# Kernel optimization log

Measured on AMD Instinct MI355X. Metric: run time of the kernel, lower is better.

The kernel has to match this reference:

```python
import jax, jax.numpy as jnp
import numpy as np

GROUPS = 3
EPS = 1e-5

def _conv(x, w, groups, pad):
    # x: NCHW, w: OIHW (grouped). pad: 'VALID' for 1x1, ((1,1),(1,1)) for 3x3 same.
    return jax.lax.conv_general_dilated(
        x, w, window_strides=(1, 1), padding=pad,
        feature_group_count=groups,
        dimension_numbers=('NCHW', 'OIHW', 'NCHW'))

def _bn(x, g, b, m, v):
    # folded inference batchnorm: y = x*scale + (beta - mean*scale)
    s = g / jnp.sqrt(v + EPS)
    return x * s[None, :, None, None] + (b - m * s)[None, :, None, None]

def _shuffle(x, groups):
    B, C, H, W = x.shape
    return x.reshape(B, groups, C // groups, H, W).transpose(0, 2, 1, 3, 4).reshape(B, C, H, W)

def setup_inputs() -> dict:
    key = jax.random.key(0)
    ks = jax.random.split(key, 16)
    B, Cin, Cout, H, W = 64, 480, 480, 28, 28
    mid = Cout // 4  # 120
    d = {}
    d['x'] = jax.random.normal(ks[0], (B, Cin, H, W), jnp.float32)
    d['w1'] = jax.random.normal(ks[1], (mid, Cin // GROUPS, 1, 1), jnp.float32) * 0.05
    d['g1'] = jax.random.uniform(ks[2], (mid,), jnp.float32)
    d['b1'] = jax.random.normal(ks[3], (mid,), jnp.float32)
    d['m1'] = jax.random.normal(ks[4], (mid,), jnp.float32)
    d['v1'] = jax.random.uniform(ks[5], (mid,), jnp.float32)
    d['w2'] = jax.random.normal(ks[6], (mid, 1, 3, 3), jnp.float32) * 0.05
    d['g2'] = jax.random.uniform(ks[7], (mid,), jnp.float32)
    d['b2'] = jax.random.normal(ks[8], (mid,), jnp.float32)
    d['m2'] = jax.random.normal(ks[9], (mid,), jnp.float32)
    d['v2'] = jax.random.uniform(ks[10], (mid,), jnp.float32)
    d['w3'] = jax.random.normal(ks[11], (Cout, mid // GROUPS, 1, 1), jnp.float32) * 0.05
    d['g3'] = jax.random.uniform(ks[12], (Cout,), jnp.float32)
    d['b3'] = jax.random.normal(ks[13], (Cout,), jnp.float32)
    d['m3'] = jax.random.normal(ks[14], (Cout,), jnp.float32)
    d['v3'] = jax.random.uniform(ks[15], (Cout,), jnp.float32)
    return d

def reference(x, w1, g1, b1, m1, v1, w2, g2, b2, m2, v2, w3, g3, b3, m3, v3):
    mid = w2.shape[0]
    shortcut = x  # in_channels == out_channels -> identity shortcut
    out = jax.nn.relu(_bn(_conv(x, w1, GROUPS, 'VALID'), g1, b1, m1, v1))
    out = _bn(_conv(out, w2, mid, ((1, 1), (1, 1))), g2, b2, m2, v2)  # depthwise 3x3
    out = _shuffle(out, GROUPS)
    out = jax.nn.relu(_bn(_conv(out, w3, GROUPS, 'VALID'), g3, b3, m3, v3))
    return out + shortcut
```

## Files before the change

### kernel.cpp

```cpp
#include <hip/hip_runtime.h>


namespace {
constexpr int CIN = 480;
constexpr int MID = 120;
constexpr int HWP = 784;
constexpr float EPSV = 1e-5f;

constexpr size_t TMP1_N   = (size_t)64 * MID * HWP;
constexpr size_t G_SHORTS = (size_t)784 * 3 * 4096;
constexpr size_t G_FLOATS = G_SHORTS / 2;
constexpr size_t PAR_OFF  = TMP1_N + G_FLOATS;
constexpr int WA1_N = 3 * 3 * 5 * 64 * 8;
constexpr int WA3_N = 3 * 10 * 2 * 64 * 8;

constexpr int S1X = 161;
constexpr int S2O = 69;
constexpr int S3O = 67;
}

typedef short bf16x8 __attribute__((ext_vector_type(8)));
typedef float f32x4  __attribute__((ext_vector_type(4)));

__device__ inline unsigned short f2bf(float v) {
    unsigned u = __float_as_uint(v);
    return (unsigned short)((u + 0x7fffu + ((u >> 16) & 1u)) >> 16);
}
__device__ inline float bf2f(unsigned short s) {
    return __uint_as_float(((unsigned)s) << 16);
}
__device__ inline void split2(float v, unsigned short& h, unsigned short& l) {
    h = f2bf(v);
    l = f2bf(v - bf2f(h));
}

__global__ __launch_bounds__(256) void prep_k(
    const float* __restrict__ w1, const float* __restrict__ w3,
    const float* __restrict__ g1, const float* __restrict__ b1,
    const float* __restrict__ m1, const float* __restrict__ v1,
    const float* __restrict__ g2, const float* __restrict__ b2,
    const float* __restrict__ m2, const float* __restrict__ v2,
    const float* __restrict__ g3, const float* __restrict__ b3,
    const float* __restrict__ m3, const float* __restrict__ v3,
    float* __restrict__ par, unsigned short* __restrict__ wpk,
    unsigned short* __restrict__ G)
{
    const int t = blockIdx.x * 256 + threadIdx.x;
    if (t < 720) {
        if (t < 120) {
            const float s = g1[t] * rsqrtf(v1[t] + EPSV);
            par[t] = s; par[120 + t] = fmaf(-m1[t], s, b1[t]);
        } else if (t < 240) {
            const int c = t - 120;
            const float s = g2[c] * rsqrtf(v2[c] + EPSV);
            par[240 + c] = s; par[360 + c] = fmaf(-m2[c], s, b2[c]);
        } else {
            const int c = t - 240;
            const float s = g3[c] * rsqrtf(v3[c] + EPSV);
            par[480 + c] = s; par[960 + c] = fmaf(-m3[c], s, b3[c]);
        }
    } else if (t < 3600) {
        const int t1   = t - 720;
        const int lane = t1 & 63;
        const int rest = t1 >> 6;
        const int ks   = rest % 5;
        const int mtg  = rest / 5;
        const int mt   = mtg % 3;
        const int g    = mtg / 3;
        const int row  = mt * 16 + (lane & 15);
        const int k0   = ks * 32 + (lane >> 4) * 8;
        unsigned short h[8], l[8];
#pragma unroll
        for (int j = 0; j < 8; ++j) {
            float v = (row < 40) ? w1[(size_t)(g * 40 + row) * 160 + k0 + j] : 0.f;
            split2(v, h[j], l[j]);
        }
        *reinterpret_cast<uint4*>(wpk + (size_t)t1 * 8)         = *reinterpret_cast<uint4*>(h);
        *reinterpret_cast<uint4*>(wpk + WA1_N + (size_t)t1 * 8) = *reinterpret_cast<uint4*>(l);
    } else if (t < 7440) {
        const int t3   = t - 3600;
        const int lane = t3 & 63;
        const int rest = t3 >> 6;
        const int ks   = rest % 2;
        const int mtg  = rest / 2;
        const int mt   = mtg % 10;
        const int g    = mtg / 10;
        const int row  = mt * 16 + (lane & 15);
        const int k0   = ks * 32 + (lane >> 4) * 8;
        unsigned short h[8], l[8];
#pragma unroll
        for (int j = 0; j < 8; ++j) {
            const int k = k0 + j;
            float v = (k < 40) ? w3[(size_t)(g * 160 + row) * 40 + k] : 0.f;
            split2(v, h[j], l[j]);
        }
        *reinterpret_cast<uint4*>(wpk + 2 * WA1_N + (size_t)t3 * 8)         = *reinterpret_cast<uint4*>(h);
        *reinterpret_cast<uint4*>(wpk + 2 * WA1_N + WA3_N + (size_t)t3 * 8) = *reinterpret_cast<uint4*>(l);
    } else {
        const int z = t - 7440;
        if (z < 451584) {
            const int tg  = z / 192;
            const int off = z - tg * 192;
            *reinterpret_cast<uint4*>(G + (size_t)tg * 4096 + 2560 + off * 8) =
                make_uint4(0u, 0u, 0u, 0u);
        }
    }
}

__global__ __launch_bounds__(256) void k1_mfma(
    const float* __restrict__ x, const unsigned short* __restrict__ wA1h,
    const float* __restrict__ par, float* __restrict__ tmp1)
{
    __shared__ float xs[64 * S1X];
    __shared__ float sL[40], shL[40];

    const int tid  = threadIdx.x;
    const int lane = tid & 63;
    const int wv   = tid >> 6;
    const int g    = blockIdx.y;
    const int p0   = blockIdx.x * 64;

    if (tid < 40) { sL[tid] = par[g * 40 + tid]; shL[tid] = par[120 + g * 40 + tid]; }

#pragma unroll
    for (int i = 0; i < 10; ++i) {
        const int task = tid + i * 256;
        const int ch   = task >> 4;
        const int px4  = task & 15;
        const int p    = p0 + px4 * 4;
        const int b    = p / HWP;
        const int hw   = p - b * HWP;
        const float4 v = *reinterpret_cast<const float4*>(
            x + ((size_t)b * CIN + g * 160 + ch) * HWP + hw);
        float* d = xs + (px4 * 4) * S1X + ch;
        d[0] = v.x; d[S1X] = v.y; d[2 * S1X] = v.z; d[3 * S1X] = v.w;
    }
    __syncthreads();

    const unsigned short* __restrict__ wA1l = wA1h + WA1_N;
    f32x4 acc[3];
#pragma unroll
    for (int mt = 0; mt < 3; ++mt) acc[mt] = f32x4{0.f, 0.f, 0.f, 0.f};

    const int n16 = lane & 15;
    const int kq  = lane >> 4;
    const int pxl = wv * 16 + n16;
#pragma unroll
    for (int ks = 0; ks < 5; ++ks) {
        const int k0 = ks * 32 + kq * 8;
        const float* bp = xs + pxl * S1X + k0;
        bf16x8 Bh, Bl;
#pragma unroll
        for (int j = 0; j < 8; ++j) {
            unsigned short h, l;
            split2(bp[j], h, l);
            Bh[j] = (short)h; Bl[j] = (short)l;
        }
#pragma unroll
        for (int mt = 0; mt < 3; ++mt) {
            const size_t fi = (((size_t)(g * 3 + mt) * 5 + ks) * 64 + lane) * 8;
            const bf16x8 Ah = *reinterpret_cast<const bf16x8*>(wA1h + fi);
            const bf16x8 Al = *reinterpret_cast<const bf16x8*>(wA1l + fi);
            acc[mt] = __builtin_amdgcn_mfma_f32_16x16x32_bf16(Ah, Bh, acc[mt], 0, 0, 0);
            acc[mt] = __builtin_amdgcn_mfma_f32_16x16x32_bf16(Ah, Bl, acc[mt], 0, 0, 0);
            acc[mt] = __builtin_amdgcn_mfma_f32_16x16x32_bf16(Al, Bh, acc[mt], 0, 0, 0);
        }
    }

    {
        int hw = (p0 % HWP) + pxl, bb = p0 / HWP;
        if (hw >= HWP) { hw -= HWP; ++bb; }
        const int rb = kq * 4;
#pragma unroll
        for (int mt = 0; mt < 3; ++mt) {
#pragma unroll
            for (int r = 0; r < 4; ++r) {
                const int ocl = mt * 16 + rb + r;
                if (ocl < 40) {
                    float val = fmaf(acc[mt][r], sL[ocl], shL[ocl]);
                    tmp1[((size_t)bb * MID + g * 40 + ocl) * HWP + hw] = val > 0.f ? val : 0.f;
                }
            }
        }
    }
}

__global__ __launch_bounds__(256) void k2_dw(
    const float* __restrict__ tmp1, const float* __restrict__ w2,
    const float* __restrict__ par, unsigned short* __restrict__ G)
{
    __shared__ float dout[MID * S2O];
    __shared__ float w2s[1080];
    __shared__ float s2s[120], sh2s[120];

    const int tid = threadIdx.x;
    const int bx  = blockIdx.x;
    const int p0  = bx * 64;

    for (int i = tid; i < 1080; i += 256) w2s[i] = w2[i];
    if (tid < 120) { s2s[tid] = par[240 + tid]; sh2s[tid] = par[360 + tid]; }
    __syncthreads();

#pragma unroll
    for (int i = 0; i < 8; ++i) {
        const int task = tid + i * 256;
        if (task < 1920) {
            const int ch  = task >> 4;
            const int px4 = task & 15;
            const int p   = p0 + px4 * 4;
            const int b   = p / HWP;
            const int hw  = p - b * HWP;
            const int h   = hw / 28, w = hw - h * 28;
            const float* __restrict__ in = tmp1 + ((size_t)b * MID + ch) * HWP;
            const float* wk = w2s + ch * 9;

            float a0 = 0.f, a1 = 0.f, a2 = 0.f, a3 = 0.f;
#pragma unroll
            for (int dh = -1; dh <= 1; ++dh) {
                const int hh = h + dh;
                if (hh < 0 || hh > 27) continue;
                const float* r = in + hh * 28 + w;
                const float4 c4 = *reinterpret_cast<const float4*>(r);
                const float cl = (w > 0)  ? r[-1] : 0.f;
                const float cr = (w < 24) ? r[4]  : 0.f;
                const float* wr = wk + (dh + 1) * 3;
                a0 = fmaf(cl,   wr[0], a0); a0 = fmaf(c4.x, wr[1], a0); a0 = fmaf(c4.y, wr[2], a0);
                a1 = fmaf(c4.x, wr[0], a1); a1 = fmaf(c4.y, wr[1], a1); a1 = fmaf(c4.z, wr[2], a1);
                a2 = fmaf(c4.y, wr[0], a2); a2 = fmaf(c4.z, wr[1], a2); a2 = fmaf(c4.w, wr[2], a2);
                a3 = fmaf(c4.z, wr[0], a3); a3 = fmaf(c4.w, wr[1], a3); a3 = fmaf(cr,   wr[2], a3);
            }
            const float s  = s2s[ch];
            const float sh = sh2s[ch];
            const int gi = ch / 40;
            const int cs = (ch - gi * 40) * 3 + gi;
            float* d = dout + cs * S2O + px4 * 4;
            d[0] = fmaf(a0, s, sh); d[1] = fmaf(a1, s, sh);
            d[2] = fmaf(a2, s, sh); d[3] = fmaf(a3, s, sh);
        }
    }
    __syncthreads();

#pragma unroll
    for (int i = 0; i < 4; ++i) {
        const int task = tid + i * 256;
        if (task < 960) {
            const int cb  = task >> 6;
            const int pxl = task & 63;
            const int cs0 = cb * 8;
            unsigned short res[8];
#pragma unroll
            for (int j = 0; j < 8; ++j)
                res[j] = f2bf(dout[(cs0 + j) * S2O + pxl]);
            const int gk  = cs0 / 40;
            const int icg = cs0 - gk * 40;
            const int kb8 = icg >> 3, ks = kb8 >> 2, kbl = kb8 & 3;
            const int nt  = pxl >> 4, n16 = pxl & 15;
            unsigned short* dst = G +
                (((((size_t)bx * 3 + gk) * 2 + ks) * 4 + kbl) * 4 + nt) * 128 + n16 * 8;
            *reinterpret_cast<uint4*>(dst) = *reinterpret_cast<uint4*>(res);
        }
    }
}

__global__ __launch_bounds__(256) void k3_mfma(
    const unsigned short* __restrict__ G, const unsigned short* __restrict__ wA3h,
    const float* __restrict__ par,
    const float* __restrict__ x, float* __restrict__ out)
{
    __shared__ float osr[80 * S3O];
    __shared__ float sL[80], shL[80];

    const int tid  = threadIdx.x;
    const int lane = tid & 63;
    const int wv   = tid >> 6;
    const int bx   = blockIdx.x;
    const int g    = blockIdx.y >> 1;
    const int mh   = blockIdx.y & 1;
    if (tid < 80) {
        sL[tid]  = par[480 + g * 160 + mh * 80 + tid];
        shL[tid] = par[960 + g * 160 + mh * 80 + tid];
    }
    __syncthreads();

    const unsigned short* __restrict__ wA3l = wA3h + WA3_N;
    const int nt = wv;
    f32x4 acc[5];
#pragma unroll
    for (int mt = 0; mt < 5; ++mt) acc[mt] = f32x4{0.f, 0.f, 0.f, 0.f};

    const int kbl = lane >> 4, n16l = lane & 15;
#pragma unroll
    for (int ks = 0; ks < 2; ++ks) {
        const bf16x8 Bv = *reinterpret_cast<const bf16x8*>(
            G + (((((size_t)bx * 3 + g) * 2 + ks) * 4 + kbl) * 4 + nt) * 128 + n16l * 8);
#pragma unroll
        for (int mt = 0; mt < 5; ++mt) {
            const size_t fi = (((size_t)(g * 10 + mh * 5 + mt) * 2 + ks) * 64 + lane) * 8;
            const bf16x8 Ah = *reinterpret_cast<const bf16x8*>(wA3h + fi);
            const bf16x8 Al = *reinterpret_cast<const bf16x8*>(wA3l + fi);
            acc[mt] = __builtin_amdgcn_mfma_f32_16x16x32_bf16(Ah, Bv, acc[mt], 0, 0, 0);
            acc[mt] = __builtin_amdgcn_mfma_f32_16x16x32_bf16(Al, Bv, acc[mt], 0, 0, 0);
        }
    }

    {
        const int n16 = lane & 15, kq = lane >> 4;
        const int pxl = nt * 16 + n16;
#pragma unroll
        for (int mt = 0; mt < 5; ++mt) {
#pragma unroll
            for (int r = 0; r < 4; ++r) {
                const int ocl = mt * 16 + kq * 4 + r;
                float val = fmaf(acc[mt][r], sL[ocl], shL[ocl]);
                osr[ocl * S3O + pxl] = val > 0.f ? val : 0.f;
            }
        }
    }
    __syncthreads();

#pragma unroll
    for (int i = 0; i < 5; ++i) {
        const int task = tid + i * 256;
        const int ocl  = task >> 4;
        const int px4  = task & 15;
        const int p    = bx * 64 + px4 * 4;
        const int b    = p / HWP;
        const int hw   = p - b * HWP;
        const int oc   = g * 160 + mh * 80 + ocl;
        const size_t idx = ((size_t)b * CIN + oc) * HWP + hw;
        const float* s = osr + ocl * S3O + px4 * 4;
        const float4 sc = *reinterpret_cast<const float4*>(x + idx);
        float4 o;
        o.x = s[0] + sc.x; o.y = s[1] + sc.y;
        o.z = s[2] + sc.z; o.w = s[3] + sc.w;
        *reinterpret_cast<float4*>(out + idx) = o;
    }
}

extern "C" void kernel_launch(void* const* d_in, const int* in_sizes, int n_in,
                              void* d_out, int out_size, void* d_ws, size_t ws_size,
                              hipStream_t stream) {
    const float* x  = (const float*)d_in[0];
    const float* w1 = (const float*)d_in[1];
    const float* g1 = (const float*)d_in[2];
    const float* b1 = (const float*)d_in[3];
    const float* m1 = (const float*)d_in[4];
    const float* v1 = (const float*)d_in[5];
    const float* w2 = (const float*)d_in[6];
    const float* g2 = (const float*)d_in[7];
    const float* b2 = (const float*)d_in[8];
    const float* m2 = (const float*)d_in[9];
    const float* v2 = (const float*)d_in[10];
    const float* w3 = (const float*)d_in[11];
    const float* g3 = (const float*)d_in[12];
    const float* b3 = (const float*)d_in[13];
    const float* m3 = (const float*)d_in[14];
    const float* v3 = (const float*)d_in[15];
    float* out = (float*)d_out;

    float* wsf = (float*)d_ws;
    float* tmp1 = wsf;
    unsigned short* G = (unsigned short*)(wsf + TMP1_N);
    float* par = wsf + PAR_OFF;
    unsigned short* wpk = (unsigned short*)(par + 1440);

    prep_k<<<1794, 256, 0, stream>>>(w1, w3, g1, b1, m1, v1, g2, b2, m2, v2,
                                     g3, b3, m3, v3, par, wpk, G);
    k1_mfma<<<dim3(784, 3), 256, 0, stream>>>(x, wpk, par, tmp1);
    k2_dw  <<<784,          256, 0, stream>>>(tmp1, w2, par, G);
    k3_mfma<<<dim3(784, 6), 256, 0, stream>>>(G, wpk + 2 * WA1_N, par, x, out);
}
```

Baseline: 105.8 us.

## Store stage-1 intermediate as bf16 and move G zeroing into depthwise kernel

```diff
diff --git a/kernel.cpp b/kernel.cpp
--- a/kernel.cpp
+++ b/kernel.cpp
@@ -15,6 +15,7 @@
 constexpr int WA3_N = 3 * 10 * 2 * 64 * 8;
 
 constexpr int S1X = 161;
+constexpr int S1O = 65;
 constexpr int S2O = 69;
 constexpr int S3O = 67;
 }
@@ -26,12 +27,17 @@
     unsigned u = __float_as_uint(v);
     return (unsigned short)((u + 0x7fffu + ((u >> 16) & 1u)) >> 16);
 }
-__device__ inline float bf2f(unsigned short s) {
-    return __uint_as_float(((unsigned)s) << 16);
+__device__ inline float bf2f(unsigned s) {
+    return __uint_as_float(s << 16);
 }
 __device__ inline void split2(float v, unsigned short& h, unsigned short& l) {
     h = f2bf(v);
     l = f2bf(v - bf2f(h));
+}
+__device__ inline unsigned pksplit(float v) {
+    unsigned short h, l;
+    split2(v, h, l);
+    return (unsigned)h | ((unsigned)l << 16);
 }
 
 __global__ __launch_bounds__(256) void prep_k(
@@ -42,8 +48,7 @@
     const float* __restrict__ m2, const float* __restrict__ v2,
     const float* __restrict__ g3, const float* __restrict__ b3,
     const float* __restrict__ m3, const float* __restrict__ v3,
-    float* __restrict__ par, unsigned short* __restrict__ wpk,
-    unsigned short* __restrict__ G)
+    float* __restrict__ par, unsigned short* __restrict__ wpk)
 {
     const int t = blockIdx.x * 256 + threadIdx.x;
     if (t < 720) {
@@ -96,22 +101,14 @@
         }
         *reinterpret_cast<uint4*>(wpk + 2 * WA1_N + (size_t)t3 * 8)         = *reinterpret_cast<uint4*>(h);
         *reinterpret_cast<uint4*>(wpk + 2 * WA1_N + WA3_N + (size_t)t3 * 8) = *reinterpret_cast<uint4*>(l);
-    } else {
-        const int z = t - 7440;
-        if (z < 451584) {
-            const int tg  = z / 192;
-            const int off = z - tg * 192;
-            *reinterpret_cast<uint4*>(G + (size_t)tg * 4096 + 2560 + off * 8) =
-                make_uint4(0u, 0u, 0u, 0u);
-        }
     }
 }
 
 __global__ __launch_bounds__(256) void k1_mfma(
     const float* __restrict__ x, const unsigned short* __restrict__ wA1h,
-    const float* __restrict__ par, float* __restrict__ tmp1)
+    const float* __restrict__ par, unsigned short* __restrict__ tmp1)
 {
-    __shared__ float xs[64 * S1X];
+    __shared__ unsigned xs[64 * S1X];
     __shared__ float sL[40], shL[40];
 
     const int tid  = threadIdx.x;
@@ -132,8 +129,11 @@
         const int hw   = p - b * HWP;
         const float4 v = *reinterpret_cast<const float4*>(
             x + ((size_t)b * CIN + g * 160 + ch) * HWP + hw);
-        float* d = xs + (px4 * 4) * S1X + ch;
-        d[0] = v.x; d[S1X] = v.y; d[2 * S1X] = v.z; d[3 * S1X] = v.w;
+        unsigned* d = xs + (px4 * 4) * S1X + ch;
+        d[0]       = pksplit(v.x);
+        d[S1X]     = pksplit(v.y);
+        d[2 * S1X] = pksplit(v.z);
+        d[3 * S1X] = pksplit(v.w);
     }
     __syncthreads();
 
@@ -147,14 +147,13 @@
     const int pxl = wv * 16 + n16;
 #pragma unroll
     for (int ks = 0; ks < 5; ++ks) {
-        const int k0 = ks * 32 + kq * 8;
-        const float* bp = xs + pxl * S1X + k0;
+        const unsigned* bp = xs + pxl * S1X + ks * 32 + kq * 8;
         bf16x8 Bh, Bl;
 #pragma unroll
         for (int j = 0; j < 8; ++j) {
-            unsigned short h, l;
-            split2(bp[j], h, l);
-            Bh[j] = (short)h; Bl[j] = (short)l;
+            const unsigned w = bp[j];
+            Bh[j] = (short)(w & 0xffffu);
+            Bl[j] = (short)(w >> 16);
         }
 #pragma unroll
         for (int mt = 0; mt < 3; ++mt) {
@@ -166,27 +165,44 @@
             acc[mt] = __builtin_amdgcn_mfma_f32_16x16x32_bf16(Al, Bh, acc[mt], 0, 0, 0);
         }
     }
-
+    __syncthreads();
+
+    float* osr = reinterpret_cast<float*>(xs);
     {
-        int hw = (p0 % HWP) + pxl, bb = p0 / HWP;
-        if (hw >= HWP) { hw -= HWP; ++bb; }
-        const int rb = kq * 4;
 #pragma unroll
         for (int mt = 0; mt < 3; ++mt) {
 #pragma unroll
             for (int r = 0; r < 4; ++r) {
-                const int ocl = mt * 16 + rb + r;
+                const int ocl = mt * 16 + kq * 4 + r;
                 if (ocl < 40) {
                     float val = fmaf(acc[mt][r], sL[ocl], shL[ocl]);
-                    tmp1[((size_t)bb * MID + g * 40 + ocl) * HWP + hw] = val > 0.f ? val : 0.f;
+                    osr[ocl * S1O + pxl] = val > 0.f ? val : 0.f;
                 }
             }
         }
     }
+    __syncthreads();
+
+#pragma unroll
+    for (int i = 0; i < 3; ++i) {
+        const int task = tid + i * 256;
+        if (task < 640) {
+            const int ocl = task >> 4;
+            const int px4 = task & 15;
+            const int p   = p0 + px4 * 4;
+            const int b   = p / HWP;
+            const int hw  = p - b * HWP;
+            const float* s = osr + ocl * S1O + px4 * 4;
+            const unsigned lo = (unsigned)f2bf(s[0]) | ((unsigned)f2bf(s[1]) << 16);
+            const unsigned hi = (unsigned)f2bf(s[2]) | ((unsigned)f2bf(s[3]) << 16);
+            *reinterpret_cast<uint2*>(
+                tmp1 + ((size_t)b * MID + g * 40 + ocl) * HWP + hw) = make_uint2(lo, hi);
+        }
+    }
 }
 
 __global__ __launch_bounds__(256) void k2_dw(
-    const float* __restrict__ tmp1, const float* __restrict__ w2,
+    const unsigned short* __restrict__ tmp1, const float* __restrict__ w2,
     const float* __restrict__ par, unsigned short* __restrict__ G)
 {
     __shared__ float dout[MID * S2O];
@@ -196,6 +212,17 @@
     const int tid = threadIdx.x;
     const int bx  = blockIdx.x;
     const int p0  = bx * 64;
+
+#pragma unroll
+    for (int i = 0; i < 3; ++i) {
+        const int task = tid + i * 256;
+        if (task < 576) {
+            const int gk  = task / 192;
+            const int off = task - gk * 192;
+            *reinterpret_cast<uint4*>(G + ((size_t)bx * 3 + gk) * 4096 + 2560 + (size_t)off * 8) =
+                make_uint4(0u, 0u, 0u, 0u);
+        }
+    }
 
     for (int i = tid; i < 1080; i += 256) w2s[i] = w2[i];
     if (tid < 120) { s2s[tid] = par[240 + tid]; sh2s[tid] = par[360 + tid]; }
@@ -211,7 +238,7 @@
             const int b   = p / HWP;
             const int hw  = p - b * HWP;
             const int h   = hw / 28, w = hw - h * 28;
-            const float* __restrict__ in = tmp1 + ((size_t)b * MID + ch) * HWP;
+            const unsigned short* __restrict__ in = tmp1 + ((size_t)b * MID + ch) * HWP;
             const float* wk = w2s + ch * 9;
 
             float a0 = 0.f, a1 = 0.f, a2 = 0.f, a3 = 0.f;
@@ -219,15 +246,17 @@
             for (int dh = -1; dh <= 1; ++dh) {
                 const int hh = h + dh;
                 if (hh < 0 || hh > 27) continue;
-                const float* r = in + hh * 28 + w;
-                const float4 c4 = *reinterpret_cast<const float4*>(r);
-                const float cl = (w > 0)  ? r[-1] : 0.f;
-                const float cr = (w < 24) ? r[4]  : 0.f;
+                const unsigned short* r = in + hh * 28 + w;
+                const uint2 cc = *reinterpret_cast<const uint2*>(r);
+                const float c0 = bf2f(cc.x & 0xffffu), c1 = bf2f(cc.x >> 16);
+                const float c2 = bf2f(cc.y & 0xffffu), c3 = bf2f(cc.y >> 16);
+                const float cl = (w > 0)  ? bf2f(r[-1]) : 0.f;
+                const float cr = (w < 24) ? bf2f(r[4])  : 0.f;
                 const float* wr = wk + (dh + 1) * 3;
-                a0 = fmaf(cl,   wr[0], a0); a0 = fmaf(c4.x, wr[1], a0); a0 = fmaf(c4.y, wr[2], a0);
-                a1 = fmaf(c4.x, wr[0], a1); a1 = fmaf(c4.y, wr[1], a1); a1 = fmaf(c4.z, wr[2], a1);
-                a2 = fmaf(c4.y, wr[0], a2); a2 = fmaf(c4.z, wr[1], a2); a2 = fmaf(c4.w, wr[2], a2);
-                a3 = fmaf(c4.z, wr[0], a3); a3 = fmaf(c4.w, wr[1], a3); a3 = fmaf(cr,   wr[2], a3);
+                a0 = fmaf(cl, wr[0], a0); a0 = fmaf(c0, wr[1], a0); a0 = fmaf(c1, wr[2], a0);
+                a1 = fmaf(c0, wr[0], a1); a1 = fmaf(c1, wr[1], a1); a1 = fmaf(c2, wr[2], a1);
+                a2 = fmaf(c1, wr[0], a2); a2 = fmaf(c2, wr[1], a2); a2 = fmaf(c3, wr[2], a2);
+                a3 = fmaf(c2, wr[0], a3); a3 = fmaf(c3, wr[1], a3); a3 = fmaf(cr, wr[2], a3);
             }
             const float s  = s2s[ch];
             const float sh = sh2s[ch];
@@ -359,13 +388,13 @@
     float* out = (float*)d_out;
 
     float* wsf = (float*)d_ws;
-    float* tmp1 = wsf;
+    unsigned short* tmp1 = (unsigned short*)wsf;
     unsigned short* G = (unsigned short*)(wsf + TMP1_N);
     float* par = wsf + PAR_OFF;
     unsigned short* wpk = (unsigned short*)(par + 1440);
 
-    prep_k<<<1794, 256, 0, stream>>>(w1, w3, g1, b1, m1, v1, g2, b2, m2, v2,
-                                     g3, b3, m3, v3, par, wpk, G);
+    prep_k<<<30, 256, 0, stream>>>(w1, w3, g1, b1, m1, v1, g2, b2, m2, v2,
+                                   g3, b3, m3, v3, par, wpk);
     k1_mfma<<<dim3(784, 3), 256, 0, stream>>>(x, wpk, par, tmp1);
     k2_dw  <<<784,          256, 0, stream>>>(tmp1, w2, par, G);
     k3_mfma<<<dim3(784, 6), 256, 0, stream>>>(G, wpk + 2 * WA1_N, par, x, out);
```

New measurement: 107.5 us. Within noise of the previous version (+1.6%).
